# Kernel tuning notes

Measured on AMD Instinct MI355X. Metric: run time of the kernel, lower is better.

The kernel has to match this reference:

```python
import jax, jax.numpy as jnp
import numpy as np

D = 512
H = 8
DH = D // H  # 64


def setup_inputs() -> dict:
    key = jax.random.key(0)
    ks = jax.random.split(key, 7)
    batch, la, lb = 8, 256, 256
    A = jax.random.normal(ks[0], (batch, la, D), dtype=jnp.float32)
    B = jax.random.normal(ks[1], (batch, lb, D), dtype=jnp.float32)
    s = 1.0 / np.sqrt(D)
    W1 = jax.random.uniform(ks[2], (D, D), minval=-s, maxval=s, dtype=jnp.float32)
    b1 = jax.random.uniform(ks[3], (D,), minval=-s, maxval=s, dtype=jnp.float32)
    W2 = jax.random.uniform(ks[4], (D, D), minval=-s, maxval=s, dtype=jnp.float32)
    b2 = jax.random.uniform(ks[5], (D,), minval=-s, maxval=s, dtype=jnp.float32)
    q = jax.random.normal(ks[6], (DH,), dtype=jnp.float32) * 0.1
    return {"A": A, "B": B, "W1": W1, "b1": b1, "W2": W2, "b2": b2, "q": q}


def reference(A, B, W1, b1, W2, b2, q):
    bs, la, _ = A.shape
    lb = B.shape[1]
    # Linear + ReLU, then raw row-major reshape to (batch, heads, len, dh)
    # (matches torch .view semantics: NOT a head-transpose split)
    A_ = jax.nn.relu(A @ W1.T + b1).reshape(bs, H, la, DH)
    B_ = jax.nn.relu(B @ W2.T + b2).reshape(bs, H, lb, DH)
    # bilinear score: tanh of elementwise pairwise product, dotted with q
    # att_maps: [bs, H, la, lb]
    att_maps = jnp.einsum(
        "bhijc,c->bhij",
        jnp.tanh(A_[:, :, :, None, :] * B_[:, :, None, :, :]),
        q,
    )
    temp_b2a = jax.nn.softmax(jnp.mean(att_maps, axis=3), axis=2)  # [bs,H,la]
    temp_a2b = jax.nn.softmax(jnp.mean(att_maps, axis=2), axis=2)  # [bs,H,lb]
    A_heads = A.reshape(bs, H, la, DH)
    B_heads = B.reshape(bs, H, lb, DH)
    A_p = jnp.sum(A_heads * temp_b2a[..., None], axis=2).reshape(bs, -1)  # [bs, d]
    B_p = jnp.sum(B_heads * temp_a2b[..., None], axis=2).reshape(bs, -1)  # [bs, d]
    return (
        jnp.concatenate((A_p, B_p), axis=1),
        jnp.mean(temp_b2a, axis=1),
        jnp.mean(temp_a2b, axis=1),
    )
```

## Files before the change

kernel.cpp:

```cpp
#include <hip/hip_runtime.h>
#include <hip/hip_bf16.h>

#define LOG2E 1.4426950408889634f
#define SC2   2.8853900817779268f

typedef __attribute__((ext_vector_type(8))) short short8b;
typedef __attribute__((ext_vector_type(4))) short short4b;
typedef __attribute__((ext_vector_type(4))) float f32x4;

__device__ __forceinline__ float fast_exp2(float x) {
#if __has_builtin(__builtin_amdgcn_exp2f)
  return __builtin_amdgcn_exp2f(x);
#else
  return exp2f(x);
#endif
}
__device__ __forceinline__ float fast_rcp(float x) {
#if __has_builtin(__builtin_amdgcn_rcpf)
  return __builtin_amdgcn_rcpf(x);
#else
  return 1.0f / x;
#endif
}
__device__ __forceinline__ short f2bf(float f) {
  __hip_bfloat16 h = __float2bfloat16(f);
  return *reinterpret_cast<short*>(&h);
}

__global__ __launch_bounds__(256) void gemm_mfma_kernel(
    const float* __restrict__ Xa, const float* __restrict__ Wa,
    const float* __restrict__ ba, float* __restrict__ Oa,
    const float* __restrict__ Xb, const float* __restrict__ Wb,
    const float* __restrict__ bb, float* __restrict__ Ob) {
  const float* X = blockIdx.z ? Xb : Xa;
  const float* W = blockIdx.z ? Wb : Wa;
  const float* bias = blockIdx.z ? bb : ba;
  float* O = blockIdx.z ? Ob : Oa;

  __shared__ __align__(16) short As[128 * 40];
  __shared__ __align__(16) short Ws[64 * 40];

  int t = threadIdx.x;
  int m0 = blockIdx.x * 128, n0 = blockIdx.y * 64;
  int l = t & 63, w = t >> 6;
  int wm = (w >> 1) * 64, wn = (w & 1) * 32;
  int lr = l & 15, ko = (l >> 4) * 8;

  f32x4 acc[4][2];
#pragma unroll
  for (int m = 0; m < 4; ++m)
#pragma unroll
    for (int n = 0; n < 2; ++n) acc[m][n] = f32x4{0.f, 0.f, 0.f, 0.f};

  for (int k0 = 0; k0 < 512; k0 += 32) {
#pragma unroll
    for (int s = 0; s < 4; ++s) {
      int slot = t + s * 256;
      int row = slot >> 3, q = (slot & 7) << 2;
      float4 v = *reinterpret_cast<const float4*>(&X[(m0 + row) * 512 + k0 + q]);
      short4b sv = {f2bf(v.x), f2bf(v.y), f2bf(v.z), f2bf(v.w)};
      *reinterpret_cast<short4b*>(&As[row * 40 + q]) = sv;
    }
#pragma unroll
    for (int s = 0; s < 2; ++s) {
      int slot = t + s * 256;
      int row = slot >> 3, q = (slot & 7) << 2;
      float4 v = *reinterpret_cast<const float4*>(&W[(n0 + row) * 512 + k0 + q]);
      short4b sv = {f2bf(v.x), f2bf(v.y), f2bf(v.z), f2bf(v.w)};
      *reinterpret_cast<short4b*>(&Ws[row * 40 + q]) = sv;
    }
    __syncthreads();

    short8b afr[4], bfr[2];
#pragma unroll
    for (int m = 0; m < 4; ++m)
      afr[m] = *reinterpret_cast<const short8b*>(&As[(wm + m * 16 + lr) * 40 + ko]);
#pragma unroll
    for (int n = 0; n < 2; ++n)
      bfr[n] = *reinterpret_cast<const short8b*>(&Ws[(wn + n * 16 + lr) * 40 + ko]);
#pragma unroll
    for (int m = 0; m < 4; ++m)
#pragma unroll
      for (int n = 0; n < 2; ++n)
        acc[m][n] = __builtin_amdgcn_mfma_f32_16x16x32_bf16(afr[m], bfr[n], acc[m][n], 0, 0, 0);
    __syncthreads();
  }

#pragma unroll
  for (int n = 0; n < 2; ++n) {
    int col = n0 + wn + n * 16 + lr;
    float bv = bias[col];
#pragma unroll
    for (int m = 0; m < 4; ++m) {
      int rbase = m0 + wm + m * 16 + (l >> 4) * 4;
#pragma unroll
      for (int r = 0; r < 4; ++r) {
        float v = acc[m][n][r] + bv;
        O[(rbase + r) * 512 + col] = v > 0.f ? v : 0.f;
      }
    }
  }
}

__global__ __launch_bounds__(256) void compact_kernel(
    const float* __restrict__ Br, const float* __restrict__ q,
    float2* __restrict__ Cb, unsigned* __restrict__ Cnt, float* __restrict__ Ksum) {
  int bh = blockIdx.x;
  int t = threadIdx.x;
  __shared__ float Bls[256 * 65];
  __shared__ float qls[64];
  const float* Bbase = Br + bh * 16384;
#pragma unroll
  for (int it = 0; it < 16; ++it) {
    int idx = it * 256 + t;
    int j = idx >> 4, c4 = (idx & 15) << 2;
    float4 v = *reinterpret_cast<const float4*>(&Bbase[j * 64 + c4]);
    Bls[j * 65 + c4 + 0] = v.x; Bls[j * 65 + c4 + 1] = v.y;
    Bls[j * 65 + c4 + 2] = v.z; Bls[j * 65 + c4 + 3] = v.w;
  }
  if (t < 64) qls[t] = q[t];
  __syncthreads();

  int j = t;
  float2* dst = Cb + (bh * 256 + j) * 64;
  int cnt = 0;
  float K = 0.f;
  for (int c = 0; c < 64; ++c) {
    float v = Bls[j * 65 + c];
    if (v > 0.f) {
      K += qls[c];
      unsigned qb = (__float_as_uint(-2.f * qls[c]) & ~63u) | (unsigned)c;
      dst[cnt] = make_float2(v * SC2, __uint_as_float(qb));
      ++cnt;
    }
  }
  while (cnt & 3) { dst[cnt] = make_float2(0.f, 0.f); ++cnt; }
  Cnt[bh * 256 + j] = (unsigned)cnt;
  Ksum[bh * 256 + j] = K;
}

__global__ __launch_bounds__(512, 6) void attmap_kernel(
    const float* __restrict__ Ar, const float2* __restrict__ Cb,
    const unsigned* __restrict__ Cnt,
    float* __restrict__ rowpart, float* __restrict__ colsum) {
  int bh = blockIdx.x, jblk = blockIdx.y, isplit = blockIdx.z;
  int t = threadIdx.x;
  int il = t & 127, g = t >> 7;
  __shared__ __align__(16) float Als[128 * 65];
  __shared__ __align__(16) float2 Pls[32 * 64];
  __shared__ unsigned cntls[32];
  __shared__ float red[512];
  __shared__ float cpart[8][8];

  const float* Abase = Ar + bh * 16384 + isplit * 8192;
#pragma unroll
  for (int it = 0; it < 4; ++it) {
    int idx = it * 512 + t;
    int r = idx >> 4, c4 = (idx & 15) << 2;
    float4 v = *reinterpret_cast<const float4*>(&Abase[r * 64 + c4]);
    Als[r * 65 + c4 + 0] = v.x; Als[r * 65 + c4 + 1] = v.y;
    Als[r * 65 + c4 + 2] = v.z; Als[r * 65 + c4 + 3] = v.w;
  }
  {
    const float4* Pb = reinterpret_cast<const float4*>(Cb + (bh * 256 + jblk * 32) * 64);
    float4* Pd = reinterpret_cast<float4*>(Pls);
#pragma unroll
    for (int it = 0; it < 2; ++it) Pd[it * 512 + t] = Pb[it * 512 + t];
  }
  if (t < 32) cntls[t] = Cnt[bh * 256 + jblk * 32 + t];
  __syncthreads();

  const float* Arow = &Als[il * 65];
  float acc[8];
#pragma unroll
  for (int jj = 0; jj < 8; ++jj) acc[jj] = 0.f;

#pragma unroll
  for (int jj = 0; jj < 8; ++jj) {
    int jl = g * 8 + jj;
    int n = (int)cntls[jl];
    const float4* P4 = reinterpret_cast<const float4*>(&Pls[jl * 64]);
    float accj = 0.f;
#pragma unroll 1
    for (int s = 0; s < n; s += 4) {
      float4 u = P4[s >> 1];
      float4 v = P4[(s >> 1) + 1];
      float a0 = Arow[__float_as_uint(u.y) & 63u];
      float a1 = Arow[__float_as_uint(u.w) & 63u];
      float a2 = Arow[__float_as_uint(v.y) & 63u];
      float a3 = Arow[__float_as_uint(v.w) & 63u];
      float e0 = fast_exp2(a0 * u.x);
      float e1 = fast_exp2(a1 * u.z);
      float e2 = fast_exp2(a2 * v.x);
      float e3 = fast_exp2(a3 * v.z);
      float r0 = fast_rcp(e0 + 1.f);
      float r1 = fast_rcp(e1 + 1.f);
      float r2 = fast_rcp(e2 + 1.f);
      float r3 = fast_rcp(e3 + 1.f);
      accj = fmaf(u.y, r0, accj);
      accj = fmaf(u.w, r1, accj);
      accj = fmaf(v.y, r2, accj);
      accj = fmaf(v.w, r3, accj);
    }
    acc[jj] = accj;
  }

  float rs = 0.f;
#pragma unroll
  for (int jj = 0; jj < 8; ++jj) rs += acc[jj];
  red[t] = rs;

  int lane = t & 63, w = t >> 6;
#pragma unroll
  for (int jj = 0; jj < 8; ++jj) {
    float v = acc[jj];
#pragma unroll
    for (int off = 32; off >= 1; off >>= 1) v += __shfl_xor(v, off);
    if (lane == 0) cpart[w][jj] = v;
  }
  __syncthreads();
  if (t < 128) {
    rowpart[(bh * 8 + jblk) * 256 + isplit * 128 + t] =
        red[t] + red[t + 128] + red[t + 256] + red[t + 384];
  } else if (t < 160) {
    int jl = t - 128;
    int gg = jl >> 3, jj = jl & 7;
    colsum[(bh * 2 + isplit) * 256 + jblk * 32 + jl] =
        cpart[2 * gg][jj] + cpart[2 * gg + 1][jj];
  }
}

__global__ __launch_bounds__(512) void softmax_pool_kernel(
    const float* __restrict__ rowpart, const float* __restrict__ colsum,
    const float* __restrict__ Ksum,
    const float* __restrict__ A0, const float* __restrict__ B0,
    float* __restrict__ b2a, float* __restrict__ a2b, float* __restrict__ out) {
  int bh = blockIdx.x;
  int b = bh >> 3, h = bh & 7;
  int t = threadIdx.x;
  int tt = t & 255;
  int lane = t & 63, w = (t >> 6) & 3;
  __shared__ float redA[4], redB[4], redC[4], redD[4];
  __shared__ float tA[256], tB[256];
  __shared__ float pp[8][64];

  float r = 0.f;
#pragma unroll
  for (int jb = 0; jb < 8; ++jb) r += rowpart[(bh * 8 + jb) * 256 + tt];
  r *= (1.f / 256.f);
  float cs = Ksum[bh * 256 + tt] +
             (colsum[(bh * 2 + 0) * 256 + tt] + colsum[(bh * 2 + 1) * 256 + tt]) * (1.f / 256.f);

  float mr = r, mc = cs;
#pragma unroll
  for (int off = 32; off >= 1; off >>= 1) {
    mr = fmaxf(mr, __shfl_xor(mr, off));
    mc = fmaxf(mc, __shfl_xor(mc, off));
  }
  if (lane == 0) { redA[w] = mr; redB[w] = mc; }
  __syncthreads();
  mr = fmaxf(fmaxf(redA[0], redA[1]), fmaxf(redA[2], redA[3]));
  mc = fmaxf(fmaxf(redB[0], redB[1]), fmaxf(redB[2], redB[3]));

  float er = fast_exp2((r - mr) * LOG2E);
  float ec = fast_exp2((cs - mc) * LOG2E);
  float sr = er, sc = ec;
#pragma unroll
  for (int off = 32; off >= 1; off >>= 1) {
    sr += __shfl_xor(sr, off);
    sc += __shfl_xor(sc, off);
  }
  if (lane == 0) { redC[w] = sr; redD[w] = sc; }
  __syncthreads();
  sr = redC[0] + redC[1] + redC[2] + redC[3];
  sc = redD[0] + redD[1] + redD[2] + redD[3];

  float vb2a = er * fast_rcp(sr);
  float va2b = ec * fast_rcp(sc);
  tA[tt] = vb2a; tB[tt] = va2b;
  b2a[bh * 256 + tt] = vb2a;
  a2b[bh * 256 + tt] = va2b;
  __syncthreads();

  int c = t & 63, iq = t >> 6;
  const float* Ab = A0 + b * 131072 + h * 16384;
  const float* Bb = B0 + b * 131072 + h * 16384;
  float pa = 0.f, pb = 0.f;
#pragma unroll 4
  for (int ii = 0; ii < 32; ++ii) {
    int i = (iq << 5) + ii;
    pa = fmaf(Ab[i * 64 + c], tA[i], pa);
    pb = fmaf(Bb[i * 64 + c], tB[i], pb);
  }
  pp[iq][c] = pa;
  __syncthreads();
  if (t < 64) {
    float s = 0.f;
#pragma unroll
    for (int k = 0; k < 8; ++k) s += pp[k][t];
    out[b * 1024 + h * 64 + t] = s;
  }
  __syncthreads();
  pp[iq][c] = pb;
  __syncthreads();
  if (t < 64) {
    float s = 0.f;
#pragma unroll
    for (int k = 0; k < 8; ++k) s += pp[k][t];
    out[b * 1024 + 512 + h * 64 + t] = s;
  }
}

__global__ __launch_bounds__(256) void mean_heads_kernel(
    const float* __restrict__ b2a, const float* __restrict__ a2b,
    float* __restrict__ out) {
  int b = blockIdx.x, t = threadIdx.x;
  float s1 = 0.f, s2 = 0.f;
#pragma unroll
  for (int h = 0; h < 8; ++h) {
    s1 += b2a[(b * 8 + h) * 256 + t];
    s2 += a2b[(b * 8 + h) * 256 + t];
  }
  out[8192 + b * 256 + t] = s1 * 0.125f;
  out[10240 + b * 256 + t] = s2 * 0.125f;
}

extern "C" void kernel_launch(void* const* d_in, const int* in_sizes, int n_in,
                              void* d_out, int out_size, void* d_ws, size_t ws_size,
                              hipStream_t stream) {
  const float* A  = (const float*)d_in[0];
  const float* B  = (const float*)d_in[1];
  const float* W1 = (const float*)d_in[2];
  const float* b1 = (const float*)d_in[3];
  const float* W2 = (const float*)d_in[4];
  const float* b2 = (const float*)d_in[5];
  const float* q  = (const float*)d_in[6];
  float* out = (float*)d_out;
  float* ws = (float*)d_ws;

  float*    Ar      = ws;
  float*    Brr     = ws + 1048576;
  float2*   Cb      = (float2*)(ws + 2097152);
  unsigned* Cnt     = (unsigned*)(ws + 4194304);
  float*    Ksum    = ws + 4210688;
  float*    rowpart = ws + 4227072;
  float*    colsum  = ws + 4358144;
  float*    b2a     = ws;
  float*    a2b     = ws + 16384;

  gemm_mfma_kernel<<<dim3(16, 8, 2), 256, 0, stream>>>(A, W1, b1, Ar, B, W2, b2, Brr);
  compact_kernel<<<64, 256, 0, stream>>>(Brr, q, Cb, Cnt, Ksum);
  attmap_kernel<<<dim3(64, 8, 2), 512, 0, stream>>>(Ar, Cb, Cnt, rowpart, colsum);
  softmax_pool_kernel<<<64, 512, 0, stream>>>(rowpart, colsum, Ksum, A, B, b2a, a2b, out);
  mean_heads_kernel<<<8, 256, 0, stream>>>(b2a, a2b, out);
}
```

Baseline: 77.76 us.

## Parallelize compaction, read packed B directly from global, pair reciprocals in attmap

The compact kernel is split across 512 blocks, with eight lanes per row and a shuffle prefix scan computing write offsets, so it no longer runs one serial loop per row on only 64 blocks. The attmap kernel drops its LDS staging of the packed B entries and counts and reads them wave-uniformly from global memory through readfirstlane. The tanh-sum inner loop combines two sigmoid terms over a common denominator, halving the reciprocal instructions, and clamps the exponent to avoid overflow. Occupancy hint raised to 8 blocks per CU via less shared memory; risks are global-load latency in the inner loop and rounding changes.

```diff
diff --git a/kernel.cpp b/kernel.cpp
--- a/kernel.cpp
+++ b/kernel.cpp
@@ -105,50 +105,74 @@
 __global__ __launch_bounds__(256) void compact_kernel(
     const float* __restrict__ Br, const float* __restrict__ q,
     float2* __restrict__ Cb, unsigned* __restrict__ Cnt, float* __restrict__ Ksum) {
-  int bh = blockIdx.x;
+  int blk = blockIdx.x;
+  int bh = blk >> 3, jblk = blk & 7;
   int t = threadIdx.x;
-  __shared__ float Bls[256 * 65];
+  int jl = t >> 3, p = t & 7;
+  __shared__ float Bls[32][65];
   __shared__ float qls[64];
-  const float* Bbase = Br + bh * 16384;
-#pragma unroll
-  for (int it = 0; it < 16; ++it) {
+
+  const float* Bbase = Br + bh * 16384 + jblk * 2048;
+#pragma unroll
+  for (int it = 0; it < 2; ++it) {
     int idx = it * 256 + t;
-    int j = idx >> 4, c4 = (idx & 15) << 2;
-    float4 v = *reinterpret_cast<const float4*>(&Bbase[j * 64 + c4]);
-    Bls[j * 65 + c4 + 0] = v.x; Bls[j * 65 + c4 + 1] = v.y;
-    Bls[j * 65 + c4 + 2] = v.z; Bls[j * 65 + c4 + 3] = v.w;
+    int row = idx >> 4, c4 = (idx & 15) << 2;
+    float4 v = *reinterpret_cast<const float4*>(&Bbase[row * 64 + c4]);
+    Bls[row][c4 + 0] = v.x; Bls[row][c4 + 1] = v.y;
+    Bls[row][c4 + 2] = v.z; Bls[row][c4 + 3] = v.w;
   }
   if (t < 64) qls[t] = q[t];
   __syncthreads();
 
-  int j = t;
-  float2* dst = Cb + (bh * 256 + j) * 64;
-  int cnt = 0;
+  int c0 = p * 8;
+  int nz = 0;
   float K = 0.f;
-  for (int c = 0; c < 64; ++c) {
-    float v = Bls[j * 65 + c];
+#pragma unroll
+  for (int cc = 0; cc < 8; ++cc) {
+    float v = Bls[jl][c0 + cc];
+    if (v > 0.f) { ++nz; K += qls[c0 + cc]; }
+  }
+  int incl = nz;
+#pragma unroll
+  for (int d = 1; d < 8; d <<= 1) {
+    int u = __shfl_up(incl, d, 8);
+    if (p >= d) incl += u;
+  }
+  int off = incl - nz;
+  int total = __shfl(incl, 7, 8);
+
+  float2* dst = Cb + (bh * 256 + jblk * 32 + jl) * 64;
+  int k = off;
+#pragma unroll
+  for (int cc = 0; cc < 8; ++cc) {
+    int c = c0 + cc;
+    float v = Bls[jl][c];
     if (v > 0.f) {
-      K += qls[c];
       unsigned qb = (__float_as_uint(-2.f * qls[c]) & ~63u) | (unsigned)c;
-      dst[cnt] = make_float2(v * SC2, __uint_as_float(qb));
-      ++cnt;
-    }
-  }
-  while (cnt & 3) { dst[cnt] = make_float2(0.f, 0.f); ++cnt; }
-  Cnt[bh * 256 + j] = (unsigned)cnt;
-  Ksum[bh * 256 + j] = K;
-}
-
-__global__ __launch_bounds__(512, 6) void attmap_kernel(
+      dst[k] = make_float2(v * SC2, __uint_as_float(qb));
+      ++k;
+    }
+  }
+#pragma unroll
+  for (int d = 1; d < 8; d <<= 1) K += __shfl_xor(K, d, 8);
+
+  if (p == 7) {
+    int cnt = total;
+    while (cnt & 3) { dst[cnt] = make_float2(0.f, 0.f); ++cnt; }
+    Cnt[bh * 256 + jblk * 32 + jl] = (unsigned)cnt;
+    Ksum[bh * 256 + jblk * 32 + jl] = K;
+  }
+}
+
+__global__ __launch_bounds__(512, 8) void attmap_kernel(
     const float* __restrict__ Ar, const float2* __restrict__ Cb,
     const unsigned* __restrict__ Cnt,
     float* __restrict__ rowpart, float* __restrict__ colsum) {
   int bh = blockIdx.x, jblk = blockIdx.y, isplit = blockIdx.z;
   int t = threadIdx.x;
-  int il = t & 127, g = t >> 7;
+  int il = t & 127;
+  int g = __builtin_amdgcn_readfirstlane(t >> 7);
   __shared__ __align__(16) float Als[128 * 65];
-  __shared__ __align__(16) float2 Pls[32 * 64];
-  __shared__ unsigned cntls[32];
   __shared__ float red[512];
   __shared__ float cpart[8][8];
 
@@ -161,25 +185,16 @@
     Als[r * 65 + c4 + 0] = v.x; Als[r * 65 + c4 + 1] = v.y;
     Als[r * 65 + c4 + 2] = v.z; Als[r * 65 + c4 + 3] = v.w;
   }
-  {
-    const float4* Pb = reinterpret_cast<const float4*>(Cb + (bh * 256 + jblk * 32) * 64);
-    float4* Pd = reinterpret_cast<float4*>(Pls);
-#pragma unroll
-    for (int it = 0; it < 2; ++it) Pd[it * 512 + t] = Pb[it * 512 + t];
-  }
-  if (t < 32) cntls[t] = Cnt[bh * 256 + jblk * 32 + t];
   __syncthreads();
 
   const float* Arow = &Als[il * 65];
   float acc[8];
-#pragma unroll
-  for (int jj = 0; jj < 8; ++jj) acc[jj] = 0.f;
 
 #pragma unroll
   for (int jj = 0; jj < 8; ++jj) {
     int jl = g * 8 + jj;
-    int n = (int)cntls[jl];
-    const float4* P4 = reinterpret_cast<const float4*>(&Pls[jl * 64]);
+    int n = (int)__builtin_amdgcn_readfirstlane(Cnt[bh * 256 + jblk * 32 + jl]);
+    const float4* P4 = reinterpret_cast<const float4*>(Cb + (bh * 256 + jblk * 32 + jl) * 64);
     float accj = 0.f;
 #pragma unroll 1
     for (int s = 0; s < n; s += 4) {
@@ -189,18 +204,17 @@
       float a1 = Arow[__float_as_uint(u.w) & 63u];
       float a2 = Arow[__float_as_uint(v.y) & 63u];
       float a3 = Arow[__float_as_uint(v.w) & 63u];
-      float e0 = fast_exp2(a0 * u.x);
-      float e1 = fast_exp2(a1 * u.z);
-      float e2 = fast_exp2(a2 * v.x);
-      float e3 = fast_exp2(a3 * v.z);
-      float r0 = fast_rcp(e0 + 1.f);
-      float r1 = fast_rcp(e1 + 1.f);
-      float r2 = fast_rcp(e2 + 1.f);
-      float r3 = fast_rcp(e3 + 1.f);
-      accj = fmaf(u.y, r0, accj);
-      accj = fmaf(u.w, r1, accj);
-      accj = fmaf(v.y, r2, accj);
-      accj = fmaf(v.w, r3, accj);
+      float e0 = fast_exp2(fminf(a0 * u.x, 60.f));
+      float e1 = fast_exp2(fminf(a1 * u.z, 60.f));
+      float e2 = fast_exp2(fminf(a2 * v.x, 60.f));
+      float e3 = fast_exp2(fminf(a3 * v.z, 60.f));
+      float u0 = e0 + 1.f, u1 = e1 + 1.f, u2 = e2 + 1.f, u3 = e3 + 1.f;
+      float n01 = fmaf(u.w, u0, u.y * u1);
+      float n23 = fmaf(v.w, u2, v.y * u3);
+      float r01 = fast_rcp(u0 * u1);
+      float r23 = fast_rcp(u2 * u3);
+      accj = fmaf(n01, r01, accj);
+      accj = fmaf(n23, r23, accj);
     }
     acc[jj] = accj;
   }
@@ -349,7 +363,7 @@
   float*    a2b     = ws + 16384;
 
   gemm_mfma_kernel<<<dim3(16, 8, 2), 256, 0, stream>>>(A, W1, b1, Ar, B, W2, b2, Brr);
-  compact_kernel<<<64, 256, 0, stream>>>(Brr, q, Cb, Cnt, Ksum);
+  compact_kernel<<<512, 256, 0, stream>>>(Brr, q, Cb, Cnt, Ksum);
   attmap_kernel<<<dim3(64, 8, 2), 512, 0, stream>>>(Ar, Cb, Cnt, rowpart, colsum);
   softmax_pool_kernel<<<64, 512, 0, stream>>>(rowpart, colsum, Ksum, A, B, b2a, a2b, out);
   mean_heads_kernel<<<8, 256, 0, stream>>>(b2a, a2b, out);
```

Measured after the change: 73.53 us. 5.4% less time.
